# Optimization experiments

Measured on AMD Instinct MI355X. Metric: run time of the kernel, lower is better.

## Reference

```python
import jax, jax.numpy as jnp
import numpy as np

LUT_DIM = 33  # classic 3D color LUT grid size


def apply_lut(LUT, img):
    """Trilinear 3D-LUT apply. LUT: [3, D, D, D] (indexed [c, b, g, r]); img: [3, H, W] in ~[0,1]."""
    D = LUT.shape[1]
    x = img * (D - 1)                                   # [3, H, W] continuous grid coords
    i0 = jnp.clip(jnp.floor(x).astype(jnp.int32), 0, D - 2)
    f = x - i0.astype(x.dtype)                          # fractional offsets
    r0, g0, b0 = i0[0], i0[1], i0[2]                    # [H, W] int indices per channel
    fr, fg, fb = f[0], f[1], f[2]

    def corner(db, dg, dr):
        # 8-corner gather: [3, H, W]
        return LUT[:, b0 + db, g0 + dg, r0 + dr]

    w000 = (1 - fb) * (1 - fg) * (1 - fr)
    w001 = (1 - fb) * (1 - fg) * fr
    w010 = (1 - fb) * fg * (1 - fr)
    w011 = (1 - fb) * fg * fr
    w100 = fb * (1 - fg) * (1 - fr)
    w101 = fb * (1 - fg) * fr
    w110 = fb * fg * (1 - fr)
    w111 = fb * fg * fr

    out = (w000 * corner(0, 0, 0) + w001 * corner(0, 0, 1)
           + w010 * corner(0, 1, 0) + w011 * corner(0, 1, 1)
           + w100 * corner(1, 0, 0) + w101 * corner(1, 0, 1)
           + w110 * corner(1, 1, 0) + w111 * corner(1, 1, 1))
    return out


def setup_inputs() -> dict:
    key = jax.random.key(0)
    k1, k2, k3, k4 = jax.random.split(key, 4)
    H, W, N = 2160, 3840, 350
    gt = jax.random.uniform(k1, (3, H, W), dtype=jnp.float32)
    # Scale LUT entries by 1/N so the unweighted sum of 350 LUTs stays in ~[0,1]
    # (keeps the second apply_lut's gather indices in-range, as a real identity-ish LUT stack would).
    lut = jax.random.uniform(k2, (2, N, 3, LUT_DIM, LUT_DIM, LUT_DIM), dtype=jnp.float32) / N
    L0 = jax.random.normal(k3, (N,), dtype=jnp.float32)
    L1 = jax.random.normal(k4, (N,), dtype=jnp.float32)
    return {"gt": gt, "lut": lut, "L0": L0, "L1": L1}


def reference(gt, lut, L0, L1):
    # NOTE: the original forward computes softmax(L0)/softmax(L1) but never uses
    # the weights: it sums the LUT slices unweighted. We reproduce that faithfully;
    # the softmaxes are dead code and omitted.
    CL0 = lut[0].sum(axis=0)          # [3, D, D, D]
    I_s = apply_lut(CL0, gt)          # [3, H, W]
    CL1 = lut[1].sum(axis=0)          # [3, D, D, D]
    I_f = apply_lut(CL1, I_s)         # [3, H, W]
    return I_f
```

## Files before the change

kernel.cpp:

```cpp
#include <hip/hip_runtime.h>

#define HW_PIX (2160 * 3840)
#define D   33
#define D2  (33 * 33)
#define D3  (33 * 33 * 33)
#define M   (3 * D3)
#define NLUT 350
#define TWO_M (2 * M)

#define PGR  (32 * 32)
#define PENT (33 * PGR)

__global__ __launch_bounds__(256) void reduce_kernel(
    const float* __restrict__ lut,
    float* __restrict__ accum)
{
    const int lane  = threadIdx.x & 63;
    const int chunk = threadIdx.x >> 6;
    const long long u = (long long)blockIdx.x * 64 + lane;

    float s = 0.0f;
    if (u < TWO_M) {
        const int h = (u >= M) ? 1 : 0;
        const long long rem = u - (long long)h * M;
        const int start = chunk * 87 + min(chunk, 2);
        const int count = 87 + (chunk < 2 ? 1 : 0);
        const float* src = lut + (long long)h * NLUT * M + rem
                               + (long long)start * M;
        #pragma unroll 8
        for (int n = 0; n < count; ++n)
            s += src[(long long)n * M];
    }

    __shared__ float red[256];
    red[threadIdx.x] = s;
    __syncthreads();
    if (threadIdx.x < 64 && u < TWO_M) {
        float t = (red[threadIdx.x] + red[threadIdx.x + 64])
                + (red[threadIdx.x + 128] + red[threadIdx.x + 192]);
        accum[u] = t;
    }
}

__global__ __launch_bounds__(256) void pack_kernel(
    const float* __restrict__ accum,
    uint4* __restrict__ packed)
{
    int t = blockIdx.x * 256 + threadIdx.x;
    if (t >= 2 * PENT) return;
    int h = t / PENT;
    int e = t - h * PENT;
    int b = e >> 10;
    int g = (e >> 5) & 31;
    int r = e & 31;

    const float* A = accum + (long long)h * M;
    unsigned q[12];
    int j = 0;
    #pragma unroll
    for (int gg = 0; gg < 2; ++gg)
        #pragma unroll
        for (int rr = 0; rr < 2; ++rr)
            #pragma unroll
            for (int c = 0; c < 3; ++c) {
                float v = A[c * D3 + (b * D + (g + gg)) * D + (r + rr)];
                v = fminf(fmaxf(v, 0.0f), 1.0f);
                q[j++] = (unsigned)(v * 1023.0f + 0.5f);
            }
    uint4 E;
    E.x = q[0] | (q[1]  << 10) | (q[2]  << 20);
    E.y = q[3] | (q[4]  << 10) | (q[5]  << 20);
    E.z = q[6] | (q[7]  << 10) | (q[8]  << 20);
    E.w = q[9] | (q[10] << 10) | (q[11] << 20);
    packed[t] = E;
}

__device__ __forceinline__ void apply_q10(const uint4* __restrict__ L,
                                          float r, float g, float b,
                                          float& outr, float& outg, float& outb)
{
    float xr = r * 32.0f, xg = g * 32.0f, xb = b * 32.0f;
    int r0 = min(max((int)floorf(xr), 0), 31);
    int g0 = min(max((int)floorf(xg), 0), 31);
    int b0 = min(max((int)floorf(xb), 0), 31);
    float fr = xr - (float)r0;
    float fg = xg - (float)g0;
    float fb = xb - (float)b0;

    int e = (b0 << 10) + (g0 << 5) + r0;
    uint4 E0 = L[e];
    uint4 E1 = L[e + PGR];

    float w00 = (1.0f - fg) * (1.0f - fr);
    float w01 = (1.0f - fg) * fr;
    float w10 = fg * (1.0f - fr);
    float w11 = fg * fr;
    float wb0 = 1.0f - fb, wb1 = fb;

    float sr, sg, sb;
    {
        float a00 = wb0 * w00, a01 = wb0 * w01, a10 = wb0 * w10, a11 = wb0 * w11;
        sr = a00 * (float)( E0.x        & 1023) + a01 * (float)( E0.y        & 1023)
           + a10 * (float)( E0.z        & 1023) + a11 * (float)( E0.w        & 1023);
        sg = a00 * (float)((E0.x >> 10) & 1023) + a01 * (float)((E0.y >> 10) & 1023)
           + a10 * (float)((E0.z >> 10) & 1023) + a11 * (float)((E0.w >> 10) & 1023);
        sb = a00 * (float)((E0.x >> 20) & 1023) + a01 * (float)((E0.y >> 20) & 1023)
           + a10 * (float)((E0.z >> 20) & 1023) + a11 * (float)((E0.w >> 20) & 1023);
    }
    {
        float a00 = wb1 * w00, a01 = wb1 * w01, a10 = wb1 * w10, a11 = wb1 * w11;
        sr += a00 * (float)( E1.x        & 1023) + a01 * (float)( E1.y        & 1023)
            + a10 * (float)( E1.z        & 1023) + a11 * (float)( E1.w        & 1023);
        sg += a00 * (float)((E1.x >> 10) & 1023) + a01 * (float)((E1.y >> 10) & 1023)
            + a10 * (float)((E1.z >> 10) & 1023) + a11 * (float)((E1.w >> 10) & 1023);
        sb += a00 * (float)((E1.x >> 20) & 1023) + a01 * (float)((E1.y >> 20) & 1023)
            + a10 * (float)((E1.z >> 20) & 1023) + a11 * (float)((E1.w >> 20) & 1023);
    }
    const float inv = 1.0f / 1023.0f;
    outr = sr * inv; outg = sg * inv; outb = sb * inv;
}

__global__ __launch_bounds__(256) void fused_apply_kernel(
    const float* __restrict__ gt,
    const uint4* __restrict__ packed,
    float* __restrict__ out)
{
    int p = blockIdx.x * 256 + threadIdx.x;
    if (p >= HW_PIX) return;

    float r = gt[p];
    float g = gt[p + HW_PIX];
    float b = gt[p + 2 * HW_PIX];

    float r1, g1, b1;
    apply_q10(packed, r, g, b, r1, g1, b1);

    float r2, g2, b2;
    apply_q10(packed + PENT, r1, g1, b1, r2, g2, b2);

    out[p]              = r2;
    out[p + HW_PIX]     = g2;
    out[p + 2 * HW_PIX] = b2;
}

extern "C" void kernel_launch(void* const* d_in, const int* in_sizes, int n_in,
                              void* d_out, int out_size, void* d_ws, size_t ws_size,
                              hipStream_t stream)
{
    const float* gt  = (const float*)d_in[0];
    const float* lut = (const float*)d_in[1];
    float* out = (float*)d_out;

    float* accum  = (float*)d_ws;
    uint4* packed = (uint4*)((char*)d_ws + 862496);

    reduce_kernel<<<dim3((TWO_M + 63) / 64), dim3(256), 0, stream>>>(lut, accum);
    pack_kernel<<<dim3((2 * PENT + 255) / 256), dim3(256), 0, stream>>>(accum, packed);
    fused_apply_kernel<<<dim3((HW_PIX + 255) / 256), dim3(256), 0, stream>>>(gt, packed, out);
}
```

Measured before the change: 554.7 us.

## Interleave b-plane cell pairs in packed LUT and widen reduce per-thread work

The packed LUT now stores both b-plane corner entries of a cell next to each other (32 bytes per cell), so the apply kernel fetches one contiguous pair instead of two loads a plane apart. This should improve cache-line locality for the scattered gathers. The reduce kernel now has each thread accumulate four output elements, giving more independent loads in flight and a quarter of the blocks. The packed table grows slightly, because b=32 planes are no longer shared between neighbouring cells, and its workspace offset moves to 1 MiB.

```diff
diff --git a/kernel.cpp b/kernel.cpp
--- a/kernel.cpp
+++ b/kernel.cpp
@@ -8,37 +8,54 @@
 #define NLUT 350
 #define TWO_M (2 * M)
 
-#define PGR  (32 * 32)
-#define PENT (33 * PGR)
+#define PIDX  (32 * 32 * 32)
+#define PU4   (PIDX * 2)
 
 __global__ __launch_bounds__(256) void reduce_kernel(
     const float* __restrict__ lut,
     float* __restrict__ accum)
 {
-    const int lane  = threadIdx.x & 63;
-    const int chunk = threadIdx.x >> 6;
-    const long long u = (long long)blockIdx.x * 64 + lane;
+    const int lane = threadIdx.x & 63;
+    const int w    = threadIdx.x >> 6;
+    const int base = blockIdx.x * 256;
+    const int start = w * 87 + min(w, 2);
+    const int count = 87 + (w < 2 ? 1 : 0);
 
-    float s = 0.0f;
-    if (u < TWO_M) {
-        const int h = (u >= M) ? 1 : 0;
-        const long long rem = u - (long long)h * M;
-        const int start = chunk * 87 + min(chunk, 2);
-        const int count = 87 + (chunk < 2 ? 1 : 0);
-        const float* src = lut + (long long)h * NLUT * M + rem
-                               + (long long)start * M;
-        #pragma unroll 8
-        for (int n = 0; n < count; ++n)
-            s += src[(long long)n * M];
+    const float* srcp[4];
+    bool valid[4];
+    #pragma unroll
+    for (int k = 0; k < 4; ++k) {
+        long long u = (long long)base + lane + 64 * k;
+        valid[k] = (u < TWO_M);
+        long long off = valid[k]
+            ? u + (u >= M ? (long long)(NLUT - 1) * M : 0LL)
+            : 0LL;
+        srcp[k] = lut + off + (long long)start * M;
     }
 
-    __shared__ float red[256];
-    red[threadIdx.x] = s;
+    float s0 = 0.f, s1 = 0.f, s2 = 0.f, s3 = 0.f;
+    #pragma unroll 4
+    for (int n = 0; n < count; ++n) {
+        long long o = (long long)n * M;
+        s0 += srcp[0][o];
+        s1 += srcp[1][o];
+        s2 += srcp[2][o];
+        s3 += srcp[3][o];
+    }
+
+    __shared__ float red[4][64][4];
+    red[w][lane][0] = s0;
+    red[w][lane][1] = s1;
+    red[w][lane][2] = s2;
+    red[w][lane][3] = s3;
     __syncthreads();
-    if (threadIdx.x < 64 && u < TWO_M) {
-        float t = (red[threadIdx.x] + red[threadIdx.x + 64])
-                + (red[threadIdx.x + 128] + red[threadIdx.x + 192]);
-        accum[u] = t;
+
+    int o = threadIdx.x;
+    if (base + o < TWO_M) {
+        int ln = o & 63, k = o >> 6;
+        float t = (red[0][ln][k] + red[1][ln][k])
+                + (red[2][ln][k] + red[3][ln][k]);
+        accum[base + o] = t;
     }
 }
 
@@ -47,37 +64,41 @@
     uint4* __restrict__ packed)
 {
     int t = blockIdx.x * 256 + threadIdx.x;
-    if (t >= 2 * PENT) return;
-    int h = t / PENT;
-    int e = t - h * PENT;
+    if (t >= 2 * PIDX) return;
+    int h = t >> 15;
+    int e = t & (PIDX - 1);
     int b = e >> 10;
     int g = (e >> 5) & 31;
     int r = e & 31;
 
     const float* A = accum + (long long)h * M;
-    unsigned q[12];
-    int j = 0;
+    uint4 E[2];
     #pragma unroll
-    for (int gg = 0; gg < 2; ++gg)
+    for (int bb = 0; bb < 2; ++bb) {
+        unsigned q[12];
+        int j = 0;
         #pragma unroll
-        for (int rr = 0; rr < 2; ++rr)
+        for (int gg = 0; gg < 2; ++gg)
             #pragma unroll
-            for (int c = 0; c < 3; ++c) {
-                float v = A[c * D3 + (b * D + (g + gg)) * D + (r + rr)];
-                v = fminf(fmaxf(v, 0.0f), 1.0f);
-                q[j++] = (unsigned)(v * 1023.0f + 0.5f);
-            }
-    uint4 E;
-    E.x = q[0] | (q[1]  << 10) | (q[2]  << 20);
-    E.y = q[3] | (q[4]  << 10) | (q[5]  << 20);
-    E.z = q[6] | (q[7]  << 10) | (q[8]  << 20);
-    E.w = q[9] | (q[10] << 10) | (q[11] << 20);
-    packed[t] = E;
+            for (int rr = 0; rr < 2; ++rr)
+                #pragma unroll
+                for (int c = 0; c < 3; ++c) {
+                    float v = A[c * D3 + ((b + bb) * D + (g + gg)) * D + (r + rr)];
+                    v = fminf(fmaxf(v, 0.0f), 1.0f);
+                    q[j++] = (unsigned)(v * 1023.0f + 0.5f);
+                }
+        E[bb].x = q[0] | (q[1]  << 10) | (q[2]  << 20);
+        E[bb].y = q[3] | (q[4]  << 10) | (q[5]  << 20);
+        E[bb].z = q[6] | (q[7]  << 10) | (q[8]  << 20);
+        E[bb].w = q[9] | (q[10] << 10) | (q[11] << 20);
+    }
+    packed[2 * t]     = E[0];
+    packed[2 * t + 1] = E[1];
 }
 
-__device__ __forceinline__ void apply_q10(const uint4* __restrict__ L,
-                                          float r, float g, float b,
-                                          float& outr, float& outg, float& outb)
+__device__ __forceinline__ void apply_q10p(const uint4* __restrict__ L,
+                                           float r, float g, float b,
+                                           float& outr, float& outg, float& outb)
 {
     float xr = r * 32.0f, xg = g * 32.0f, xb = b * 32.0f;
     int r0 = min(max((int)floorf(xr), 0), 31);
@@ -87,9 +108,9 @@
     float fg = xg - (float)g0;
     float fb = xb - (float)b0;
 
-    int e = (b0 << 10) + (g0 << 5) + r0;
-    uint4 E0 = L[e];
-    uint4 E1 = L[e + PGR];
+    int idx = (b0 << 10) + (g0 << 5) + r0;
+    uint4 E0 = L[2 * idx];
+    uint4 E1 = L[2 * idx + 1];
 
     float w00 = (1.0f - fg) * (1.0f - fr);
     float w01 = (1.0f - fg) * fr;
@@ -133,10 +154,10 @@
     float b = gt[p + 2 * HW_PIX];
 
     float r1, g1, b1;
-    apply_q10(packed, r, g, b, r1, g1, b1);
+    apply_q10p(packed, r, g, b, r1, g1, b1);
 
     float r2, g2, b2;
-    apply_q10(packed + PENT, r1, g1, b1, r2, g2, b2);
+    apply_q10p(packed + PU4, r1, g1, b1, r2, g2, b2);
 
     out[p]              = r2;
     out[p + HW_PIX]     = g2;
@@ -152,9 +173,9 @@
     float* out = (float*)d_out;
 
     float* accum  = (float*)d_ws;
-    uint4* packed = (uint4*)((char*)d_ws + 862496);
+    uint4* packed = (uint4*)((char*)d_ws + (1 << 20));
 
-    reduce_kernel<<<dim3((TWO_M + 63) / 64), dim3(256), 0, stream>>>(lut, accum);
-    pack_kernel<<<dim3((2 * PENT + 255) / 256), dim3(256), 0, stream>>>(accum, packed);
+    reduce_kernel<<<dim3((TWO_M + 255) / 256), dim3(256), 0, stream>>>(lut, accum);
+    pack_kernel<<<dim3((2 * PIDX + 255) / 256), dim3(256), 0, stream>>>(accum, packed);
     fused_apply_kernel<<<dim3((HW_PIX + 255) / 256), dim3(256), 0, stream>>>(gt, packed, out);
 }
```

After: 546.2 us. No clear change (-1.5%).
